# Kernel tuning notes

Measured on AMD Instinct MI355X. Metric: run time of the kernel, lower is better.

Reference implementation:

```python
import jax, jax.numpy as jnp
import numpy as np

N, E = 50000, 1600000
D_IN, D_OUT = 256, 64
ALPHA = 0.2        # LeakyReLU slope used on attention logits (self.leakyrelu)
BT_SLOPE = 0.01    # F.leaky_relu default slope inside relu_bt


def _xavier_normal(key, shape, gain):
    fan_in, fan_out = shape[0], shape[1]
    std = gain * np.sqrt(2.0 / (fan_in + fan_out))
    return jax.random.normal(key, shape, dtype=jnp.float32) * std


def relu_bt(x):
    # -threshold(-leaky_relu(x), -t, -t) == min(leaky_relu(x), t), t = ||x||_inf (detached)
    t = jax.lax.stop_gradient(jnp.max(jnp.abs(x)))
    y = jnp.where(x >= 0, x, BT_SLOPE * x)
    return jnp.minimum(y, t)


def setup_inputs() -> dict:
    key = jax.random.key(0)
    k0, k1, k2, k3, k4, k5 = jax.random.split(key, 6)
    inp = jax.random.normal(k0, (N, D_IN), dtype=jnp.float32)
    edge = jax.random.randint(k1, (2, E), 0, N, dtype=jnp.int64)
    W_high = _xavier_normal(k2, (D_IN, D_OUT), 1.414)
    W_low = _xavier_normal(k3, (D_IN, D_OUT), 1.414)
    a_high = _xavier_normal(k4, (1, D_OUT), 1.414)
    a_low = _xavier_normal(k5, (1, D_OUT), 1.414)
    return {"input": inp, "edge": edge, "W_high": W_high, "W_low": W_low,
            "a_high": a_high, "a_low": a_low}


def reference(input, edge, W_high, W_low, a_high, a_low):
    n = input.shape[0]
    src, dst = edge[0], edge[1]

    h_high = relu_bt(input @ W_high)  # [N, D_OUT]
    h_low = relu_bt(input @ W_low)    # [N, D_OUT]

    # a @ (h[src] -/+ h[dst])^T == (a.h)[src] -/+ (a.h)[dst]: compute per-node scalar
    # projections first, then gather scalars per edge (avoids [E, D_OUT] edge features).
    s_high = h_high @ a_high[0]       # [N]
    s_low = h_low @ a_low[0]          # [N]

    def lrelu(x):
        return jnp.where(x >= 0, x, ALPHA * x)

    edge_e_high = jnp.exp(-lrelu(s_high[src] - s_high[dst]))  # [E]
    edge_e_low = jnp.exp(-lrelu(s_low[src] + s_low[dst]))     # [E]
    # dropout p=0.0 -> identity

    # sparse A @ ones -> per-row sum of attention weights
    rowsum_high = jax.ops.segment_sum(edge_e_high, src, num_segments=n)[:, None]
    rowsum_low = jax.ops.segment_sum(edge_e_low, src, num_segments=n)[:, None]

    # sparse A @ h -> weighted aggregation of neighbor features
    hp_high = jax.ops.segment_sum(edge_e_high[:, None] * h_high[dst], src, num_segments=n)
    hp_low = jax.ops.segment_sum(edge_e_low[:, None] * h_low[dst], src, num_segments=n)

    hp_high = hp_high / (rowsum_high + 1e-16)
    hp_low = hp_low / (rowsum_low + 1e-16)

    # concat=True branch
    return relu_bt(jnp.concatenate([hp_high, hp_low], axis=1))  # [N, 2*D_OUT]
```

## Files before the change

### kernel.cpp

```cpp
#include <hip/hip_runtime.h>
#include <hip/hip_bf16.h>
#include <cstdint>

#define NN    50000
#define NE    1600000
#define DIN   256
#define DOUT  64

#define BKT   196
#define BCAP  10240
#define EPB   8192
#define EPT   32
#define NBIN  196
#define MTB   64
#define NGEMM 782
#define SCAP  1536

typedef __attribute__((ext_vector_type(8))) short frag8;
typedef __attribute__((ext_vector_type(4))) float fragc;

union PK { __hip_bfloat162 b2; uint32_t u; };
union CH { frag8 v; uint32_t u[4]; };

__device__ __forceinline__ float leaky01(float x) { return x >= 0.f ? x : 0.01f * x; }

__device__ __forceinline__ uint32_t pk2(float lo, float hi) {
  PK p; p.b2 = __float22bfloat162_rn(make_float2(lo, hi)); return p.u;
}

__device__ __forceinline__ int   bcast_i(int v, int lane) {
  return __builtin_amdgcn_readlane(v, lane);
}
__device__ __forceinline__ float bcast_f(float v, int lane) {
  return __int_as_float(__builtin_amdgcn_readlane(__float_as_int(v), lane));
}

__device__ __forceinline__ float bfH(uint32_t u) { return __uint_as_float(u << 16); }
__device__ __forceinline__ float bfL(uint32_t u) { return __uint_as_float(u & 0xffff0000u); }

__global__ __launch_bounds__(256) void prep_kernel(
    const float* __restrict__ Wh, const float* __restrict__ Wl,
    __hip_bfloat16* __restrict__ Wt, int* __restrict__ cursor)
{
  if (blockIdx.x == 0 && threadIdx.x < BKT) cursor[threadIdx.x] = 0;
  int g = blockIdx.x * 256 + threadIdx.x;
  if (g < 2 * DOUT * DIN) {
    int m = g >> 14, rem = g & 16383;
    int n = rem >> 8, k = rem & 255;
    float v = (m ? Wl : Wh)[k * DOUT + n];
    Wt[g] = __float2bfloat16(v);
  }
}

__global__ __launch_bounds__(256) void fused_kernel(
    const float* __restrict__ inp, const __hip_bfloat16* __restrict__ Wt,
    const float* __restrict__ ah, const float* __restrict__ al,
    const int* __restrict__ edge, int* __restrict__ cursor,
    uint32_t* __restrict__ binned, uint32_t* __restrict__ HL,
    float2* __restrict__ ss)
{
  __shared__ __align__(16) char smem[45056];

  const int idx = blockIdx.x;
  const int t = threadIdx.x;

  if (idx < NBIN) {
    uint32_t* stage = (uint32_t*)smem;
    int* hist4 = (int*)(smem + 32768);
    int* cur4  = (int*)(smem + 36864);
    int* histT = (int*)(smem + 40960);
    int* scn   = (int*)(smem + 41984);
    int* sexc  = (int*)(smem + 43008);
    int* bg    = (int*)(smem + 44032);

    const int w = t >> 6;
    const int e0 = idx * EPB;
    uint32_t v[EPT];
#pragma unroll
    for (int i = 0; i < EPT; i++) {
      int e = e0 + i * 256 + t;
      if (e < NE) {
        v[i] = ((uint32_t)edge[e] << 16) | (uint32_t)edge[NE + e];
      } else {
        v[i] = 0xFFFFFFFFu;
      }
    }
    hist4[t] = 0; hist4[256 + t] = 0; hist4[512 + t] = 0; hist4[768 + t] = 0;
    cur4[t]  = 0; cur4[256 + t]  = 0; cur4[512 + t]  = 0; cur4[768 + t]  = 0;
    __syncthreads();
#pragma unroll
    for (int i = 0; i < EPT; i++) {
      int b = v[i] >> 24;
      if (b < BKT) atomicAdd(&hist4[(w << 8) + b], 1);
    }
    __syncthreads();
    {
      int h0 = hist4[t], h1 = hist4[256 + t], h2 = hist4[512 + t], h3 = hist4[768 + t];
      hist4[t] = 0; hist4[256 + t] = h0; hist4[512 + t] = h0 + h1; hist4[768 + t] = h0 + h1 + h2;
      int hb = h0 + h1 + h2 + h3;
      histT[t] = hb;
      scn[t] = hb;
    }
    __syncthreads();
    for (int off = 1; off < 256; off <<= 1) {
      int vv = scn[t] + ((t >= off) ? scn[t - off] : 0);
      __syncthreads();
      scn[t] = vv;
      __syncthreads();
    }
    {
      sexc[t] = scn[t] - histT[t];
      bg[t] = histT[t] ? atomicAdd(&cursor[t], histT[t]) : 0;
    }
    __syncthreads();
#pragma unroll
    for (int i = 0; i < EPT; i++) {
      int b = v[i] >> 24;
      if (b < BKT) {
        int pos = atomicAdd(&cur4[(w << 8) + b], 1);
        stage[sexc[b] + hist4[(w << 8) + b] + pos] = v[i];
      }
    }
    __syncthreads();
    const int total = scn[255];
    for (int i = t; i < total; i += 256) {
      uint32_t vv = stage[i];
      int lo = vv >> 24;
      int ofs = bg[lo] + (i - sexc[lo]);
      if (ofs < BCAP) binned[(size_t)lo * BCAP + ofs] = vv;
    }
    return;
  }

  frag8* asmem = (frag8*)smem;
  const int gid = idx - NBIN;
  const int n0 = gid * MTB;
  const int lane = t & 63;
  const int w = t >> 6;
  const int quad = lane >> 4, nn = lane & 15;

  const float4* inp4 = (const float4*)inp;
#pragma unroll
  for (int i = 0; i < 8; i++) {
    int c = i * 256 + t;
    int r = c & 15;
    int cc = c >> 4;
    int qd = cc & 3;
    int wq = cc >> 2;
    int row = ((wq >> 3) << 4) + r;
    int k0 = ((wq & 7) << 5) + (qd << 3);
    int node = n0 + row;
    float4 a0 = make_float4(0.f, 0.f, 0.f, 0.f), a1 = a0;
    if (node < NN) {
      a0 = inp4[(size_t)node * 64 + (k0 >> 2)];
      a1 = inp4[(size_t)node * 64 + (k0 >> 2) + 1];
    }
    CH ch;
    ch.u[0] = pk2(a0.x, a0.y);
    ch.u[1] = pk2(a0.z, a0.w);
    ch.u[2] = pk2(a1.x, a1.y);
    ch.u[3] = pk2(a1.z, a1.w);
    asmem[c] = ch.v;
  }
  __syncthreads();

  fragc accH[4], accL[4];
#pragma unroll
  for (int c = 0; c < 4; c++) {
    accH[c] = (fragc){0.f, 0.f, 0.f, 0.f};
    accL[c] = (fragc){0.f, 0.f, 0.f, 0.f};
  }

  const frag8* Wt8 = (const frag8*)Wt;
#pragma unroll
  for (int q = 0; q < 8; q++) {
    frag8 af = asmem[(w << 9) + (q << 6) + lane];
#pragma unroll
    for (int c = 0; c < 4; c++) {
      frag8 bh = Wt8[(c * 16 + nn) * 32 + q * 4 + quad];
      frag8 bl = Wt8[(64 + c * 16 + nn) * 32 + q * 4 + quad];
      accH[c] = __builtin_amdgcn_mfma_f32_16x16x32_bf16(af, bh, accH[c], 0, 0, 0);
      accL[c] = __builtin_amdgcn_mfma_f32_16x16x32_bf16(af, bl, accL[c], 0, 0, 0);
    }
  }

  float ahv[4], alv[4];
#pragma unroll
  for (int c = 0; c < 4; c++) { ahv[c] = ah[c * 16 + nn]; alv[c] = al[c * 16 + nn]; }
#pragma unroll
  for (int r = 0; r < 4; r++) {
    int node = n0 + (w << 4) + (quad << 2) + r;
    float sH = 0.f, sL = 0.f;
#pragma unroll
    for (int c = 0; c < 4; c++) {
      float hH = leaky01(accH[c][r]);
      float hL = leaky01(accL[c][r]);
      if (node < NN) HL[(size_t)node * DOUT + c * 16 + nn] = pk2(hH, hL);
      sH += hH * ahv[c];
      sL += hL * alv[c];
    }
#pragma unroll
    for (int off = 1; off < 16; off <<= 1) {
      sH += __shfl_xor(sH, off);
      sL += __shfl_xor(sL, off);
    }
    if (nn == 0 && node < NN) ss[node] = make_float2(sH, sL);
  }
}

__global__ __launch_bounds__(256) void agg_kernel(
    const uint32_t* __restrict__ binned, const int* __restrict__ cursor,
    const uint32_t* __restrict__ HL, const float2* __restrict__ ss,
    float* __restrict__ out)
{
  __shared__ uint32_t stg[SCAP];
  __shared__ int cnt[32], cur[32], scn[32], stt[32];
  const int b = blockIdx.x >> 3, sub = blockIdx.x & 7;
  const int t = threadIdx.x;
  if (t < 32) { cnt[t] = 0; cur[t] = 0; }
  __syncthreads();
  int nE = cursor[b]; if (nE > BCAP) nE = BCAP;
  const uint32_t* eb = binned + (size_t)b * BCAP;

  for (int i = t; i < nE; i += 256) {
    uint32_t v = eb[i];
    int loc = (v >> 16) & 255;
    if ((loc >> 5) == sub) atomicAdd(&cnt[loc & 31], 1);
  }
  __syncthreads();
  if (t < 32) scn[t] = cnt[t];
  __syncthreads();
  for (int off = 1; off < 32; off <<= 1) {
    int vv = 0;
    if (t < 32) vv = scn[t] + ((t >= off) ? scn[t - off] : 0);
    __syncthreads();
    if (t < 32) scn[t] = vv;
    __syncthreads();
  }
  if (t < 32) stt[t] = scn[t] - cnt[t];
  __syncthreads();
  for (int i = t; i < nE; i += 256) {
    uint32_t v = eb[i];
    int loc = (v >> 16) & 255;
    if ((loc >> 5) == sub) {
      int l = loc & 31;
      int pos = atomicAdd(&cur[l], 1);
      int o = stt[l] + pos;
      if (o < SCAP) stg[o] = v;
    }
  }
  __syncthreads();

  const int w = t >> 6, lane = t & 63;
  for (int i = 0; i < 8; i++) {
    int l = (w << 3) + i;
    int node = (b << 8) + (sub << 5) + l;
    if (node >= NN) continue;
    int d = cnt[l];
    int st = stt[l];
    if (st + d > SCAP) d = SCAP - st;
    if (d < 0) d = 0;
    float2 sn = ss[node];

    float accH = 0.f, accL = 0.f, rsH = 0.f, rsL = 0.f;
    for (int base = 0; base < d; base += 64) {
      int m = d - base; if (m > 64) m = 64;
      int   dst_l = 0;
      float eh_l = 0.f, el_l = 0.f;
      if (lane < m) {
        dst_l = stg[st + base + lane] & 0xffff;
        float2 sd = ss[dst_l];
        float xh = sn.x - sd.x;
        xh = (xh >= 0.f) ? xh : 0.2f * xh;
        eh_l = __expf(-xh);
        float xl = sn.y + sd.y;
        xl = (xl >= 0.f) ? xl : 0.2f * xl;
        el_l = __expf(-xl);
      }
      int j = 0;
      for (; j + 8 <= m; j += 8) {
        uint32_t u[8]; float eh[8], el[8];
#pragma unroll
        for (int x = 0; x < 8; x++) {
          int dd = bcast_i(dst_l, j + x);
          u[x]  = HL[((uint32_t)dd << 6) + lane];
          eh[x] = bcast_f(eh_l, j + x);
          el[x] = bcast_f(el_l, j + x);
        }
#pragma unroll
        for (int x = 0; x < 8; x++) {
          accH += eh[x] * bfH(u[x]); accL += el[x] * bfL(u[x]);
          rsH += eh[x]; rsL += el[x];
        }
      }
      for (; j < m; j++) {
        int      dst = bcast_i(dst_l, j);
        float    eh  = bcast_f(eh_l, j);
        float    el  = bcast_f(el_l, j);
        uint32_t u   = HL[((uint32_t)dst << 6) + lane];
        accH += eh * bfH(u);
        accL += el * bfL(u);
        rsH += eh;
        rsL += el;
      }
    }

    float oh = accH / (rsH + 1e-16f);
    float ol = accL / (rsL + 1e-16f);
    out[(size_t)node * 128 + lane]      = leaky01(oh);
    out[(size_t)node * 128 + 64 + lane] = leaky01(ol);
  }
}

extern "C" void kernel_launch(void* const* d_in, const int* in_sizes, int n_in,
                              void* d_out, int out_size, void* d_ws, size_t ws_size,
                              hipStream_t stream) {
  const float* inp  = (const float*)d_in[0];
  const int*   edge = (const int*)d_in[1];
  const float* Wh   = (const float*)d_in[2];
  const float* Wl   = (const float*)d_in[3];
  const float* ah   = (const float*)d_in[4];
  const float* al   = (const float*)d_in[5];
  float* out = (float*)d_out;

  char* ws = (char*)d_ws;
  uint32_t* HL     = (uint32_t*)(ws + 0);
  float2*   ss     = (float2*)  (ws + 12800000);
  uint32_t* binned = (uint32_t*)(ws + 13200000);
  int*      cursor = (int*)     (ws + 21228160);
  __hip_bfloat16* Wt = (__hip_bfloat16*)(ws + 21229184);

  prep_kernel<<<128, 256, 0, stream>>>(Wh, Wl, Wt, cursor);
  fused_kernel<<<NBIN + NGEMM, 256, 0, stream>>>(inp, Wt, ah, al, edge,
                                                 cursor, binned, HL, ss);
  agg_kernel<<<BKT * 8, 256, 0, stream>>>(binned, cursor, HL, ss, out);
}
```

Measured before the change: 231.1 us.

## Split aggregation into CSR build kernel with precomputed edge weights

Adds a csr_kernel that sorts each bucket's edges by local row once, computes the attention weights and row sums, and stores compact destination indices and bf16-packed weights. Previously every one of the eight sub-blocks per bucket rescanned the whole bucket. The aggregation kernel then just reads row offsets and weights, with no exp or rowsum work. The binning stage also gets half-size chunks (more blocks, less shared memory). Costs are an extra kernel launch, more workspace traffic, bf16 precision on the weights, and degree clamped to 255.

```diff
diff --git a/kernel.cpp b/kernel.cpp
--- a/kernel.cpp
+++ b/kernel.cpp
@@ -9,12 +9,12 @@
 
 #define BKT   196
 #define BCAP  10240
-#define EPB   8192
-#define EPT   32
-#define NBIN  196
+#define EPB   4096
+#define EPT   16
+#define NBIN  391
 #define MTB   64
 #define NGEMM 782
-#define SCAP  1536
+#define NAGG  1568
 
 typedef __attribute__((ext_vector_type(8))) short frag8;
 typedef __attribute__((ext_vector_type(4))) float fragc;
@@ -30,9 +30,6 @@
 
 __device__ __forceinline__ int   bcast_i(int v, int lane) {
   return __builtin_amdgcn_readlane(v, lane);
-}
-__device__ __forceinline__ float bcast_f(float v, int lane) {
-  return __int_as_float(__builtin_amdgcn_readlane(__float_as_int(v), lane));
 }
 
 __device__ __forceinline__ float bfH(uint32_t u) { return __uint_as_float(u << 16); }
@@ -42,7 +39,7 @@
     const float* __restrict__ Wh, const float* __restrict__ Wl,
     __hip_bfloat16* __restrict__ Wt, int* __restrict__ cursor)
 {
-  if (blockIdx.x == 0 && threadIdx.x < BKT) cursor[threadIdx.x] = 0;
+  if (blockIdx.x == 0 && threadIdx.x < 256) cursor[threadIdx.x] = 0;
   int g = blockIdx.x * 256 + threadIdx.x;
   if (g < 2 * DOUT * DIN) {
     int m = g >> 14, rem = g & 16383;
@@ -59,19 +56,19 @@
     uint32_t* __restrict__ binned, uint32_t* __restrict__ HL,
     float2* __restrict__ ss)
 {
-  __shared__ __align__(16) char smem[45056];
+  __shared__ __align__(16) char smem[32768];
 
   const int idx = blockIdx.x;
   const int t = threadIdx.x;
 
   if (idx < NBIN) {
     uint32_t* stage = (uint32_t*)smem;
-    int* hist4 = (int*)(smem + 32768);
-    int* cur4  = (int*)(smem + 36864);
-    int* histT = (int*)(smem + 40960);
-    int* scn   = (int*)(smem + 41984);
-    int* sexc  = (int*)(smem + 43008);
-    int* bg    = (int*)(smem + 44032);
+    int* hist4 = (int*)(smem + 16384);
+    int* cur4  = (int*)(smem + 20480);
+    int* histT = (int*)(smem + 24576);
+    int* scn   = (int*)(smem + 25600);
+    int* sexc  = (int*)(smem + 26624);
+    int* bg    = (int*)(smem + 27648);
 
     const int w = t >> 6;
     const int e0 = idx * EPB;
@@ -208,105 +205,135 @@
   }
 }
 
-__global__ __launch_bounds__(256) void agg_kernel(
+__global__ __launch_bounds__(1024) void csr_kernel(
     const uint32_t* __restrict__ binned, const int* __restrict__ cursor,
-    const uint32_t* __restrict__ HL, const float2* __restrict__ ss,
-    float* __restrict__ out)
+    const float2* __restrict__ ss, uint16_t* __restrict__ dstS,
+    uint32_t* __restrict__ wS, uint32_t* __restrict__ rowinfo,
+    float2* __restrict__ rs)
 {
-  __shared__ uint32_t stg[SCAP];
-  __shared__ int cnt[32], cur[32], scn[32], stt[32];
-  const int b = blockIdx.x >> 3, sub = blockIdx.x & 7;
+  __shared__ float2 ssl[256];
+  __shared__ int cnt[256], cur[256], stt[256], scn[256];
+  __shared__ float rsH[256], rsL[256];
+  const int b = blockIdx.x;
   const int t = threadIdx.x;
-  if (t < 32) { cnt[t] = 0; cur[t] = 0; }
+  if (t < 256) {
+    cnt[t] = 0; cur[t] = 0; rsH[t] = 0.f; rsL[t] = 0.f;
+    int node = (b << 8) + t;
+    ssl[t] = (node < NN) ? ss[node] : make_float2(0.f, 0.f);
+  }
   __syncthreads();
   int nE = cursor[b]; if (nE > BCAP) nE = BCAP;
   const uint32_t* eb = binned + (size_t)b * BCAP;
 
-  for (int i = t; i < nE; i += 256) {
-    uint32_t v = eb[i];
-    int loc = (v >> 16) & 255;
-    if ((loc >> 5) == sub) atomicAdd(&cnt[loc & 31], 1);
-  }
-  __syncthreads();
-  if (t < 32) scn[t] = cnt[t];
-  __syncthreads();
-  for (int off = 1; off < 32; off <<= 1) {
+  uint32_t v[10], wv[10];
+#pragma unroll
+  for (int i = 0; i < 10; i++) {
+    int e = i * 1024 + t;
+    v[i] = (e < nE) ? eb[e] : 0xFFFFFFFFu;
+  }
+#pragma unroll
+  for (int i = 0; i < 10; i++) {
+    if (v[i] != 0xFFFFFFFFu) {
+      int loc = (v[i] >> 16) & 255;
+      int dst = v[i] & 0xffff;
+      float2 sd = ss[dst];
+      float2 sl = ssl[loc];
+      float xh = sl.x - sd.x;
+      xh = (xh >= 0.f) ? xh : 0.2f * xh;
+      float eh = __expf(-xh);
+      float xl = sl.y + sd.y;
+      xl = (xl >= 0.f) ? xl : 0.2f * xl;
+      float el = __expf(-xl);
+      wv[i] = pk2(eh, el);
+      atomicAdd(&cnt[loc], 1);
+      atomicAdd(&rsH[loc], eh);
+      atomicAdd(&rsL[loc], el);
+    }
+  }
+  __syncthreads();
+  if (t < 256) scn[t] = cnt[t];
+  __syncthreads();
+  for (int off = 1; off < 256; off <<= 1) {
     int vv = 0;
-    if (t < 32) vv = scn[t] + ((t >= off) ? scn[t - off] : 0);
-    __syncthreads();
-    if (t < 32) scn[t] = vv;
-    __syncthreads();
-  }
-  if (t < 32) stt[t] = scn[t] - cnt[t];
-  __syncthreads();
-  for (int i = t; i < nE; i += 256) {
-    uint32_t v = eb[i];
-    int loc = (v >> 16) & 255;
-    if ((loc >> 5) == sub) {
-      int l = loc & 31;
-      int pos = atomicAdd(&cur[l], 1);
-      int o = stt[l] + pos;
-      if (o < SCAP) stg[o] = v;
-    }
-  }
-  __syncthreads();
-
+    if (t < 256) vv = scn[t] + ((t >= off) ? scn[t - off] : 0);
+    __syncthreads();
+    if (t < 256) scn[t] = vv;
+    __syncthreads();
+  }
+  if (t < 256) stt[t] = scn[t] - cnt[t];
+  __syncthreads();
+#pragma unroll
+  for (int i = 0; i < 10; i++) {
+    if (v[i] != 0xFFFFFFFFu) {
+      int loc = (v[i] >> 16) & 255;
+      int pos = atomicAdd(&cur[loc], 1);
+      size_t o = (size_t)b * BCAP + stt[loc] + pos;
+      dstS[o] = (uint16_t)(v[i] & 0xffff);
+      wS[o] = wv[i];
+    }
+  }
+  __syncthreads();
+  if (t < 256) {
+    int node = (b << 8) + t;
+    if (node < NN) {
+      int c = cnt[t]; if (c > 255) c = 255;
+      rowinfo[node] = ((uint32_t)(b * BCAP + stt[t]) << 8) | (uint32_t)c;
+      rs[node] = make_float2(rsH[t], rsL[t]);
+    }
+  }
+}
+
+__global__ __launch_bounds__(256) void agg_kernel(
+    const uint16_t* __restrict__ dstS, const uint32_t* __restrict__ wS,
+    const uint32_t* __restrict__ rowinfo, const float2* __restrict__ rs,
+    const uint32_t* __restrict__ HL, float* __restrict__ out)
+{
+  const int t = threadIdx.x;
   const int w = t >> 6, lane = t & 63;
+  const int node0 = blockIdx.x * 32 + w * 8;
+
   for (int i = 0; i < 8; i++) {
-    int l = (w << 3) + i;
-    int node = (b << 8) + (sub << 5) + l;
+    int node = node0 + i;
     if (node >= NN) continue;
-    int d = cnt[l];
-    int st = stt[l];
-    if (st + d > SCAP) d = SCAP - st;
-    if (d < 0) d = 0;
-    float2 sn = ss[node];
-
-    float accH = 0.f, accL = 0.f, rsH = 0.f, rsL = 0.f;
+    uint32_t ri = rowinfo[node];
+    int d = ri & 255;
+    size_t ofs = ri >> 8;
+    float2 rsv = rs[node];
+
+    float accH = 0.f, accL = 0.f;
     for (int base = 0; base < d; base += 64) {
       int m = d - base; if (m > 64) m = 64;
-      int   dst_l = 0;
-      float eh_l = 0.f, el_l = 0.f;
+      int dst_l = 0, w_l = 0;
       if (lane < m) {
-        dst_l = stg[st + base + lane] & 0xffff;
-        float2 sd = ss[dst_l];
-        float xh = sn.x - sd.x;
-        xh = (xh >= 0.f) ? xh : 0.2f * xh;
-        eh_l = __expf(-xh);
-        float xl = sn.y + sd.y;
-        xl = (xl >= 0.f) ? xl : 0.2f * xl;
-        el_l = __expf(-xl);
+        dst_l = dstS[ofs + base + lane];
+        w_l   = (int)wS[ofs + base + lane];
       }
       int j = 0;
       for (; j + 8 <= m; j += 8) {
-        uint32_t u[8]; float eh[8], el[8];
+        uint32_t u[8]; uint32_t ww[8];
 #pragma unroll
         for (int x = 0; x < 8; x++) {
           int dd = bcast_i(dst_l, j + x);
+          ww[x] = (uint32_t)bcast_i(w_l, j + x);
           u[x]  = HL[((uint32_t)dd << 6) + lane];
-          eh[x] = bcast_f(eh_l, j + x);
-          el[x] = bcast_f(el_l, j + x);
         }
 #pragma unroll
         for (int x = 0; x < 8; x++) {
-          accH += eh[x] * bfH(u[x]); accL += el[x] * bfL(u[x]);
-          rsH += eh[x]; rsL += el[x];
+          accH += bfH(ww[x]) * bfH(u[x]);
+          accL += bfL(ww[x]) * bfL(u[x]);
         }
       }
       for (; j < m; j++) {
-        int      dst = bcast_i(dst_l, j);
-        float    eh  = bcast_f(eh_l, j);
-        float    el  = bcast_f(el_l, j);
-        uint32_t u   = HL[((uint32_t)dst << 6) + lane];
-        accH += eh * bfH(u);
-        accL += el * bfL(u);
-        rsH += eh;
-        rsL += el;
-      }
-    }
-
-    float oh = accH / (rsH + 1e-16f);
-    float ol = accL / (rsL + 1e-16f);
+        int dd = bcast_i(dst_l, j);
+        uint32_t wwx = (uint32_t)bcast_i(w_l, j);
+        uint32_t u = HL[((uint32_t)dd << 6) + lane];
+        accH += bfH(wwx) * bfH(u);
+        accL += bfL(wwx) * bfL(u);
+      }
+    }
+
+    float oh = accH / (rsv.x + 1e-16f);
+    float ol = accL / (rsv.y + 1e-16f);
     out[(size_t)node * 128 + lane]      = leaky01(oh);
     out[(size_t)node * 128 + 64 + lane] = leaky01(ol);
   }
@@ -324,14 +351,19 @@
   float* out = (float*)d_out;
 
   char* ws = (char*)d_ws;
-  uint32_t* HL     = (uint32_t*)(ws + 0);
-  float2*   ss     = (float2*)  (ws + 12800000);
-  uint32_t* binned = (uint32_t*)(ws + 13200000);
-  int*      cursor = (int*)     (ws + 21228160);
+  uint32_t* HL      = (uint32_t*)(ws + 0);
+  float2*   ss      = (float2*)  (ws + 12800000);
+  uint32_t* binned  = (uint32_t*)(ws + 13200000);
+  int*      cursor  = (int*)     (ws + 21228160);
   __hip_bfloat16* Wt = (__hip_bfloat16*)(ws + 21229184);
+  uint32_t* wS      = (uint32_t*)(ws + 21294720);
+  uint16_t* dstS    = (uint16_t*)(ws + 29322880);
+  uint32_t* rowinfo = (uint32_t*)(ws + 33336960);
+  float2*   rs      = (float2*)  (ws + 33536960);
 
   prep_kernel<<<128, 256, 0, stream>>>(Wh, Wl, Wt, cursor);
   fused_kernel<<<NBIN + NGEMM, 256, 0, stream>>>(inp, Wt, ah, al, edge,
                                                  cursor, binned, HL, ss);
-  agg_kernel<<<BKT * 8, 256, 0, stream>>>(binned, cursor, HL, ss, out);
-}
+  csr_kernel<<<BKT, 1024, 0, stream>>>(binned, cursor, ss, dstS, wS, rowinfo, rs);
+  agg_kernel<<<NAGG, 256, 0, stream>>>(dstS, wS, rowinfo, rs, HL, out);
+}
```

After: 237.3 us. +2.7%, slower.
